# Kernel optimization log

Measured on AMD Instinct MI355X. Metric: run time of the kernel, lower is better.

The kernel has to match this reference:

```python
import jax, jax.numpy as jnp
import numpy as np

B, S, R, C = 1, 256, 256, 256   # batch, sequence_num, sequence_size, channel_size_msa
H, D = 8, 32                     # nhead, hidden_channel
EPS = 1e-5


def setup_inputs() -> dict:
    key = jax.random.key(0)
    ks = jax.random.split(key, 6)
    sd = 0.02
    return {
        "msa_repr": jax.random.normal(ks[0], (B, S, R, C), jnp.float32),
        "ln_w": jnp.ones((S,), jnp.float32),
        "ln_b": jnp.zeros((S,), jnp.float32),
        "Wq": jax.random.normal(ks[1], (C, H * D), jnp.float32) * sd,
        "Wk": jax.random.normal(ks[2], (C, H * D), jnp.float32) * sd,
        "Wv": jax.random.normal(ks[3], (C, H * D), jnp.float32) * sd,
        "Wg": jax.random.normal(ks[4], (C, H * D), jnp.float32) * sd,
        "bg": jnp.zeros((H * D,), jnp.float32),
        "Wo": jax.random.normal(ks[5], (H * D, C), jnp.float32) * sd,
        "bo": jnp.zeros((C,), jnp.float32),
    }


def reference(msa_repr, ln_w, ln_b, Wq, Wk, Wv, Wg, bg, Wo, bo):
    b, s, r, c = msa_repr.shape
    # [b, s, r, c] -> [b, r, s, c]: attention runs across sequences (column-wise)
    x = jnp.transpose(msa_repr, (0, 2, 1, 3))
    # LayerNorm over the s (sequence_num) axis, weight/bias indexed by s
    mu = jnp.mean(x, axis=2, keepdims=True)
    var = jnp.var(x, axis=2, keepdims=True)
    x = (x - mu) / jnp.sqrt(var + EPS)
    x = x * ln_w[None, None, :, None] + ln_b[None, None, :, None]
    x = x.reshape(b * r, s, c)  # flatten residue columns into batch

    q = (x @ Wq).reshape(b * r, s, H, D)
    k = (x @ Wk).reshape(b * r, s, H, D)
    v = (x @ Wv).reshape(b * r, s, H, D)
    g = jax.nn.sigmoid(x @ Wg + bg).reshape(b * r, s, H, D)

    scale = 1.0 / np.sqrt(D).astype(np.float32)
    logits = jnp.einsum('bihd,bjhd->bhij', q, k) * scale  # [(b r), H, s, s]
    attn = jax.nn.softmax(logits, axis=-1)
    out = jnp.einsum('bhij,bjhd->bihd', attn, v)           # [(b r), s, H, D]
    out = (g * out).reshape(b * r, s, H * D)
    out = out @ Wo + bo                                    # [(b r), s, c]
    out = out.reshape(b, r, s, c)
    return jnp.transpose(out, (0, 2, 1, 3))                # [b, s, r, c]
```

## Files before the change

kernel.cpp:

```cpp
#include <hip/hip_runtime.h>
#include <hip/hip_bf16.h>


using f32x4  = __attribute__((ext_vector_type(4))) float;
using bf16x8 = __attribute__((ext_vector_type(8))) short;

struct U4x { unsigned a0, a1, a2, a3; };
static_assert(sizeof(U4x) == sizeof(bf16x8), "frag size");

__device__ __forceinline__ f32x4 mfma16(bf16x8 a, bf16x8 b, f32x4 c){
  return __builtin_amdgcn_mfma_f32_16x16x32_bf16(a, b, c, 0, 0, 0);
}
__device__ __forceinline__ unsigned f2bf(float f){
  unsigned u = __builtin_bit_cast(unsigned, f);
  u += 0x7fffu + ((u >> 16) & 1u);
  return u >> 16;
}
__device__ __forceinline__ unsigned pk2(float lo, float hi){
  return f2bf(lo) | (f2bf(hi) << 16);
}
__device__ __forceinline__ bf16x8 mk_frag(unsigned a0, unsigned a1, unsigned a2, unsigned a3){
  U4x t{a0, a1, a2, a3};
  return __builtin_bit_cast(bf16x8, t);
}
__device__ __forceinline__ float sigm(float x){ return 1.f / (1.f + __expf(-x)); }

__device__ __forceinline__ int xaddr(int row, int cbyte){
  return (row << 9) + (cbyte ^ ((row & 15) << 4));
}
__device__ __forceinline__ bf16x8 lds_frag(const char* sm, int row, int cshort){
  return *(const bf16x8*)(sm + xaddr(row, cshort * 2));
}
__device__ __forceinline__ bf16x8 ldg_frag(const short* base, int row, int cshort){
  return *(const bf16x8*)(base + row * 256 + cshort);
}

__global__ __launch_bounds__(256) void prep_weights(
    const float* __restrict__ Wq, const float* __restrict__ Wk,
    const float* __restrict__ Wv, const float* __restrict__ Wg,
    const float* __restrict__ Wo, short* __restrict__ ws)
{
  const int n = blockIdx.x, t = threadIdx.x;
  ws[0*65536 + n*256 + t] = (short)f2bf(Wq[t*256 + n]);
  ws[1*65536 + n*256 + t] = (short)f2bf(Wk[t*256 + n]);
  ws[2*65536 + n*256 + t] = (short)f2bf(Wv[t*256 + n]);
  ws[3*65536 + n*256 + t] = (short)f2bf(Wg[t*256 + n]);
  ws[4*65536 + n*256 + t] = (short)f2bf(Wo[t*256 + n]);
}

__device__ __forceinline__ void build_x_tile_512(
    char* sm, const float* msa_r, const float* lnw, const float* lnb, int tid)
{
  float* muA = (float*)(sm + 131072);
  float* rsA = muA + 256;
  {
    float s0 = 0.f, s1 = 0.f;
    const int c = tid & 255, sh = tid >> 8;
    const float* p = msa_r + (sh * 128) * 65536 + c;
    #pragma unroll 8
    for (int i = 0; i < 128; i++){ float v = p[i * 65536]; s0 += v; s1 += v * v; }
    float* sb = (float*)sm;
    sb[tid] = s0; sb[512 + tid] = s1;
    __syncthreads();
    if (tid < 256){
      float tot = sb[tid] + sb[256 + tid];
      float sq  = sb[512 + tid] + sb[768 + tid];
      float mu  = tot * (1.f / 256.f);
      float var = fmaxf(sq * (1.f / 256.f) - mu * mu, 0.f);
      muA[tid] = mu; rsA[tid] = rsqrtf(var + 1e-5f);
    }
    __syncthreads();
  }
  {
    const int c0 = (tid & 31) * 8;
    float mu0[8], rs0[8];
    #pragma unroll
    for (int k = 0; k < 8; k++){ mu0[k] = muA[c0 + k]; rs0[k] = rsA[c0 + k]; }
    for (int itr = 0; itr < 16; itr++){
      const int s = itr * 16 + (tid >> 5);
      const float w = lnw[s], b = lnb[s];
      const float* rp = msa_r + s * 65536 + c0;
      f32x4 v0 = *(const f32x4*)rp;
      f32x4 v1 = *(const f32x4*)(rp + 4);
      U4x q{pk2((v0.x-mu0[0])*rs0[0]*w+b, (v0.y-mu0[1])*rs0[1]*w+b),
            pk2((v0.z-mu0[2])*rs0[2]*w+b, (v0.w-mu0[3])*rs0[3]*w+b),
            pk2((v1.x-mu0[4])*rs0[4]*w+b, (v1.y-mu0[5])*rs0[5]*w+b),
            pk2((v1.z-mu0[6])*rs0[6]*w+b, (v1.w-mu0[7])*rs0[7]*w+b)};
      *(U4x*)(sm + xaddr(s, c0 * 2)) = q;
    }
    __syncthreads();
  }
}

__global__ __launch_bounds__(512) void msa_qkvg(
    const float* __restrict__ msa, const float* __restrict__ lnw,
    const float* __restrict__ lnb, const float* __restrict__ bg,
    const short* __restrict__ wsW,
    uint4* __restrict__ kvF, uint2* __restrict__ qF, uint4* __restrict__ gF)
{
  extern __shared__ __align__(16) char sm[];
  const int r   = blockIdx.x;
  const int tid = threadIdx.x;
  build_x_tile_512(sm, msa + r * 256, lnw, lnb, tid);

  const int wid  = tid >> 6;
  const int lane = tid & 63;
  const int g = lane >> 4, c15 = lane & 15;
  const short* WqT = wsW;
  const short* WkT = wsW + 65536;
  const short* WvT = wsW + 2 * 65536;
  const short* WgT = wsW + 3 * 65536;
  const int hbase = wid * 32;
  const float bg0 = bg[hbase + c15], bg1 = bg[hbase + 16 + c15];
  const float scl = 0.17677669529663687f * 1.4426950408889634f;
  const f32x4 zz{0.f, 0.f, 0.f, 0.f};

  #pragma unroll 1
  for (int jt = 0; jt < 8; jt++){
    const int jb = jt * 32;
    f32x4 kt00=zz, kt01=zz, kt10=zz, kt11=zz;
    f32x4 va00=zz, va01=zz, va10=zz, va11=zz;
    #pragma unroll
    for (int kk = 0; kk < 8; kk++){
      const int cs = 32*kk + 8*g;
      bf16x8 wk0 = ldg_frag(WkT, hbase + c15,      cs);
      bf16x8 wk1 = ldg_frag(WkT, hbase + 16 + c15, cs);
      bf16x8 wv0 = ldg_frag(WvT, hbase + c15,      cs);
      bf16x8 wv1 = ldg_frag(WvT, hbase + 16 + c15, cs);
      bf16x8 bx0 = lds_frag(sm, jb + c15,      cs);
      bf16x8 bx1 = lds_frag(sm, jb + 16 + c15, cs);
      kt00 = mfma16(wk0, bx0, kt00);
      kt01 = mfma16(wk0, bx1, kt01);
      kt10 = mfma16(wk1, bx0, kt10);
      kt11 = mfma16(wk1, bx1, kt11);
      va00 = mfma16(bx0, wv0, va00);
      va01 = mfma16(bx0, wv1, va01);
      va10 = mfma16(bx1, wv0, va10);
      va11 = mfma16(bx1, wv1, va11);
    }
    const bf16x8 kf0 = mk_frag(pk2(kt00.x,kt00.y), pk2(kt00.z,kt00.w),
                               pk2(kt10.x,kt10.y), pk2(kt10.z,kt10.w));
    const bf16x8 kf1 = mk_frag(pk2(kt01.x,kt01.y), pk2(kt01.z,kt01.w),
                               pk2(kt11.x,kt11.y), pk2(kt11.z,kt11.w));
    const bf16x8 vf0 = mk_frag(pk2(va00.x,va00.y), pk2(va00.z,va00.w),
                               pk2(va10.x,va10.y), pk2(va10.z,va10.w));
    const bf16x8 vf1 = mk_frag(pk2(va01.x,va01.y), pk2(va01.z,va01.w),
                               pk2(va11.x,va11.y), pk2(va11.z,va11.w));
    const size_t kb = ((size_t)(r*64 + wid*8 + jt) * 4) * 64 + lane;
    kvF[kb      ] = __builtin_bit_cast(uint4, kf0);
    kvF[kb +  64] = __builtin_bit_cast(uint4, kf1);
    kvF[kb + 128] = __builtin_bit_cast(uint4, vf0);
    kvF[kb + 192] = __builtin_bit_cast(uint4, vf1);
  }

  #pragma unroll 1
  for (int dr = 0; dr < 2; dr++){
    bf16x8 wq[8];
    #pragma unroll
    for (int kk = 0; kk < 8; kk++) wq[kk] = ldg_frag(WqT, hbase + 16*dr + c15, 32*kk + 8*g);
    #pragma unroll 1
    for (int it = 0; it < 16; it++){
      f32x4 a = zz;
      #pragma unroll
      for (int kk = 0; kk < 8; kk++)
        a = mfma16(wq[kk], lds_frag(sm, it*16 + c15, 32*kk + 8*g), a);
      uint2 qv; qv.x = pk2(a.x*scl, a.y*scl); qv.y = pk2(a.z*scl, a.w*scl);
      qF[(((size_t)(r*8 + wid)*16 + it)*2 + dr)*64 + lane] = qv;
    }
  }

  #pragma unroll 1
  for (int dr = 0; dr < 2; dr++){
    bf16x8 wg[8];
    #pragma unroll
    for (int kk = 0; kk < 8; kk++) wg[kk] = ldg_frag(WgT, hbase + 16*dr + c15, 32*kk + 8*g);
    const float bgd = dr ? bg1 : bg0;
    #pragma unroll 1
    for (int it = 0; it < 16; it++){
      f32x4 a = zz;
      #pragma unroll
      for (int kk = 0; kk < 8; kk++)
        a = mfma16(lds_frag(sm, it*16 + c15, 32*kk + 8*g), wg[kk], a);
      f32x4 ga; ga.x = sigm(a.x + bgd); ga.y = sigm(a.y + bgd);
      ga.z = sigm(a.z + bgd); ga.w = sigm(a.w + bgd);
      gF[(((size_t)(r*8 + wid)*16 + it)*2 + dr)*64 + lane] = __builtin_bit_cast(uint4, ga);
    }
  }
}

__global__ __launch_bounds__(256) void msa_flash(
    const uint4* __restrict__ kvF, const uint2* __restrict__ qF,
    const uint4* __restrict__ gF, short* __restrict__ go)
{
  const int wid  = threadIdx.x >> 6;
  const int lane = threadIdx.x & 63;
  const int g = lane >> 4, c15 = lane & 15;
  const int w   = blockIdx.x * 4 + wid;
  const int r   = w >> 5;
  const int rem = w & 31;
  const int h   = rem >> 2;
  const int chq = rem & 3;
  const int hbase = h * 32;
  const int ib = chq * 64;
  const f32x4 zz{0.f, 0.f, 0.f, 0.f};

  bf16x8 bSq[4];
  #pragma unroll
  for (int nt = 0; nt < 4; nt++){
    const size_t qb = (((size_t)(r*8 + h)*16 + (ib >> 4) + nt)*2)*64 + lane;
    uint2 qlo = qF[qb], qhi = qF[qb + 64];
    bSq[nt] = mk_frag(qlo.x, qlo.y, qhi.x, qhi.y);
  }

  float l_[4];
  f32x4 o_[4][2];
  #pragma unroll
  for (int i2 = 0; i2 < 4; i2++){ l_[i2] = 0.f; o_[i2][0] = zz; o_[i2][1] = zz; }

  #pragma unroll 2
  for (int jt = 0; jt < 8; jt++){
    const size_t kb = ((size_t)(r*64 + h*8 + jt) * 4) * 64 + lane;
    const bf16x8 kf0 = __builtin_bit_cast(bf16x8, kvF[kb      ]);
    const bf16x8 kf1 = __builtin_bit_cast(bf16x8, kvF[kb +  64]);
    const bf16x8 vf0 = __builtin_bit_cast(bf16x8, kvF[kb + 128]);
    const bf16x8 vf1 = __builtin_bit_cast(bf16x8, kvF[kb + 192]);
    #pragma unroll
    for (int it = 0; it < 4; it++){
      f32x4 s0 = mfma16(kf0, bSq[it], zz);
      f32x4 s1 = mfma16(kf1, bSq[it], zz);
      float e0=exp2f(s0.x), e1=exp2f(s0.y), e2=exp2f(s0.z), e3=exp2f(s0.w);
      float e4=exp2f(s1.x), e5=exp2f(s1.y), e6=exp2f(s1.z), e7=exp2f(s1.w);
      l_[it] += ((e0+e1)+(e2+e3)) + ((e4+e5)+(e6+e7));
      bf16x8 aP = mk_frag(pk2(e0,e1), pk2(e2,e3), pk2(e4,e5), pk2(e6,e7));
      o_[it][0] = mfma16(aP, vf0, o_[it][0]);
      o_[it][1] = mfma16(aP, vf1, o_[it][1]);
    }
  }

  short* goR = go + (size_t)r * 65536;
  #pragma unroll
  for (int dr = 0; dr < 2; dr++){
    #pragma unroll
    for (int nt = 0; nt < 4; nt++){
      f32x4 ga = __builtin_bit_cast(f32x4,
          gF[(((size_t)(r*8 + h)*16 + (ib >> 4) + nt)*2 + dr)*64 + lane]);
      float lt = l_[nt];
      lt += __shfl_xor(lt, 16); lt += __shfl_xor(lt, 32);
      float inv[4];
      #pragma unroll
      for (int jj = 0; jj < 4; jj++) inv[jj] = 1.f / __shfl(lt, 4*g + jj);
      const f32x4 ov = o_[nt][dr];
      const unsigned w0 = pk2(ov[0]*inv[0]*ga.x, ov[1]*inv[1]*ga.y);
      const unsigned w1 = pk2(ov[2]*inv[2]*ga.z, ov[3]*inv[3]*ga.w);
      short* gp = goR + (ib + nt*16 + 4*g) * 256 + hbase + 16*dr + c15;
      gp[0]   = (short)(w0 & 0xffffu);
      gp[256] = (short)(w0 >> 16);
      gp[512] = (short)(w1 & 0xffffu);
      gp[768] = (short)(w1 >> 16);
    }
  }
}

__global__ __launch_bounds__(256) void out_proj(
    const short* __restrict__ go, const short* __restrict__ WoT,
    const float* __restrict__ bo, float* __restrict__ out)
{
  const int blk = blockIdx.x;
  const int r = blk >> 2, chunk = blk & 3;
  const int wid = threadIdx.x >> 6, lane = threadIdx.x & 63;
  const int g = lane >> 4, c15 = lane & 15;
  const int it = chunk * 4 + wid;
  const short* goR = go + (size_t)r * 65536;

  bf16x8 aGO[8];
  #pragma unroll
  for (int kk = 0; kk < 8; kk++) aGO[kk] = ldg_frag(goR, it*16 + c15, 32*kk + 8*g);
  #pragma unroll 2
  for (int ct = 0; ct < 16; ct++){
    f32x4 acc{0,0,0,0};
    #pragma unroll
    for (int kk = 0; kk < 8; kk++)
      acc = mfma16(aGO[kk], ldg_frag(WoT, ct*16 + c15, 32*kk + 8*g), acc);
    const float bov = bo[ct*16 + c15];
    const int i0 = it*16 + g*4;
    const int cc = ct*16 + c15;
    out[(i0 + 0) * 65536 + r * 256 + cc] = acc.x + bov;
    out[(i0 + 1) * 65536 + r * 256 + cc] = acc.y + bov;
    out[(i0 + 2) * 65536 + r * 256 + cc] = acc.z + bov;
    out[(i0 + 3) * 65536 + r * 256 + cc] = acc.w + bov;
  }
}

__global__ __launch_bounds__(512) void msa_attn_go(
    const float* __restrict__ msa, const float* __restrict__ lnw,
    const float* __restrict__ lnb, const float* __restrict__ bg,
    const short* __restrict__ wsW, short* __restrict__ go)
{
  extern __shared__ __align__(16) char sm[];
  const int r   = blockIdx.x;
  const int tid = threadIdx.x;
  build_x_tile_512(sm, msa + r * 256, lnw, lnb, tid);

  const int wid  = tid >> 6;
  const int lane = tid & 63;
  const int g = lane >> 4, c15 = lane & 15;
  const short* WqT = wsW;
  const short* WkT = wsW + 65536;
  const short* WvT = wsW + 2 * 65536;
  const short* WgT = wsW + 3 * 65536;
  const int hbase = wid * 32;
  const float bg0 = bg[hbase + c15], bg1 = bg[hbase + 16 + c15];
  const float scl = 0.17677669529663687f * 1.4426950408889634f;
  const f32x4 zz{0.f, 0.f, 0.f, 0.f};
  short* goR = go + r * 65536;

  #pragma unroll 1
  for (int chq = 0; chq < 4; chq++){
    const int ib = chq * 64;
    unsigned qTa[4][2], qTb[4][2];
    #pragma unroll
    for (int dr = 0; dr < 2; dr++){
      bf16x8 wq[8];
      #pragma unroll
      for (int kk = 0; kk < 8; kk++) wq[kk] = ldg_frag(WqT, hbase + 16*dr + c15, 32*kk + 8*g);
      #pragma unroll
      for (int nt = 0; nt < 4; nt++){
        f32x4 a = zz;
        #pragma unroll
        for (int kk = 0; kk < 8; kk++)
          a = mfma16(wq[kk], lds_frag(sm, ib + nt*16 + c15, 32*kk + 8*g), a);
        if (dr == 0){ qTa[nt][0] = pk2(a.x*scl, a.y*scl); qTa[nt][1] = pk2(a.z*scl, a.w*scl); }
        else        { qTb[nt][0] = pk2(a.x*scl, a.y*scl); qTb[nt][1] = pk2(a.z*scl, a.w*scl); }
      }
    }
    float l_[4];
    f32x4 o_[4][2];
    #pragma unroll
    for (int i2 = 0; i2 < 4; i2++){ l_[i2] = 0.f; o_[i2][0] = zz; o_[i2][1] = zz; }
    #pragma unroll 1
    for (int jt = 0; jt < 8; jt++){
      const int jb = jt * 32;
      f32x4 kt00=zz, kt01=zz, kt10=zz, kt11=zz;
      f32x4 va00=zz, va01=zz, va10=zz, va11=zz;
      #pragma unroll
      for (int kk = 0; kk < 8; kk++){
        const int cs = 32*kk + 8*g;
        bf16x8 wk0 = ldg_frag(WkT, hbase + c15,      cs);
        bf16x8 wk1 = ldg_frag(WkT, hbase + 16 + c15, cs);
        bf16x8 wv0 = ldg_frag(WvT, hbase + c15,      cs);
        bf16x8 wv1 = ldg_frag(WvT, hbase + 16 + c15, cs);
        bf16x8 bx0 = lds_frag(sm, jb + c15,      cs);
        bf16x8 bx1 = lds_frag(sm, jb + 16 + c15, cs);
        kt00 = mfma16(wk0, bx0, kt00);
        kt01 = mfma16(wk0, bx1, kt01);
        kt10 = mfma16(wk1, bx0, kt10);
        kt11 = mfma16(wk1, bx1, kt11);
        va00 = mfma16(bx0, wv0, va00);
        va01 = mfma16(bx0, wv1, va01);
        va10 = mfma16(bx1, wv0, va10);
        va11 = mfma16(bx1, wv1, va11);
      }
      const bf16x8 kf0 = mk_frag(pk2(kt00.x,kt00.y), pk2(kt00.z,kt00.w),
                                 pk2(kt10.x,kt10.y), pk2(kt10.z,kt10.w));
      const bf16x8 kf1 = mk_frag(pk2(kt01.x,kt01.y), pk2(kt01.z,kt01.w),
                                 pk2(kt11.x,kt11.y), pk2(kt11.z,kt11.w));
      const bf16x8 vf0 = mk_frag(pk2(va00.x,va00.y), pk2(va00.z,va00.w),
                                 pk2(va10.x,va10.y), pk2(va10.z,va10.w));
      const bf16x8 vf1 = mk_frag(pk2(va01.x,va01.y), pk2(va01.z,va01.w),
                                 pk2(va11.x,va11.y), pk2(va11.z,va11.w));
      #pragma unroll
      for (int it = 0; it < 4; it++){
        bf16x8 bS = mk_frag(qTa[it][0], qTa[it][1], qTb[it][0], qTb[it][1]);
        f32x4 s0 = mfma16(kf0, bS, zz);
        f32x4 s1 = mfma16(kf1, bS, zz);
        float e0=exp2f(s0.x), e1=exp2f(s0.y), e2=exp2f(s0.z), e3=exp2f(s0.w);
        float e4=exp2f(s1.x), e5=exp2f(s1.y), e6=exp2f(s1.z), e7=exp2f(s1.w);
        l_[it] += ((e0+e1)+(e2+e3)) + ((e4+e5)+(e6+e7));
        bf16x8 aP = mk_frag(pk2(e0,e1), pk2(e2,e3), pk2(e4,e5), pk2(e6,e7));
        o_[it][0] = mfma16(aP, vf0, o_[it][0]);
        o_[it][1] = mfma16(aP, vf1, o_[it][1]);
      }
    }
    #pragma unroll
    for (int dr = 0; dr < 2; dr++){
      const float bgd = dr ? bg1 : bg0;
      #pragma unroll
      for (int nt = 0; nt < 4; nt++){
        f32x4 a = zz;
        #pragma unroll
        for (int kk = 0; kk < 8; kk++)
          a = mfma16(lds_frag(sm, ib + nt*16 + c15, 32*kk + 8*g),
                     ldg_frag(WgT, hbase + 16*dr + c15, 32*kk + 8*g), a);
        float lt = l_[nt];
        lt += __shfl_xor(lt, 16); lt += __shfl_xor(lt, 32);
        float inv[4];
        #pragma unroll
        for (int jj = 0; jj < 4; jj++) inv[jj] = 1.f / __shfl(lt, 4*g + jj);
        const float ga0 = sigm(a.x + bgd), ga1 = sigm(a.y + bgd);
        const float ga2 = sigm(a.z + bgd), ga3 = sigm(a.w + bgd);
        const f32x4 ov = o_[nt][dr];
        const unsigned w0 = pk2(ov[0]*inv[0]*ga0, ov[1]*inv[1]*ga1);
        const unsigned w1 = pk2(ov[2]*inv[2]*ga2, ov[3]*inv[3]*ga3);
        short* gp = goR + (ib + nt*16 + 4*g) * 256 + hbase + 16*dr + c15;
        gp[0]   = (short)(w0 & 0xffffu);
        gp[256] = (short)(w0 >> 16);
        gp[512] = (short)(w1 & 0xffffu);
        gp[768] = (short)(w1 >> 16);
      }
    }
  }
}

extern "C" void kernel_launch(void* const* d_in, const int* in_sizes, int n_in,
                              void* d_out, int out_size, void* d_ws, size_t ws_size,
                              hipStream_t stream)
{
  (void)in_sizes; (void)n_in; (void)out_size;
  const float* msa = (const float*)d_in[0];
  const float* lnw = (const float*)d_in[1];
  const float* lnb = (const float*)d_in[2];
  const float* Wq  = (const float*)d_in[3];
  const float* Wk  = (const float*)d_in[4];
  const float* Wv  = (const float*)d_in[5];
  const float* Wg  = (const float*)d_in[6];
  const float* bg  = (const float*)d_in[7];
  const float* Wo  = (const float*)d_in[8];
  const float* bo  = (const float*)d_in[9];
  short* ws = (short*)d_ws;
  char* base = (char*)d_ws;

  prep_weights<<<256, 256, 0, stream>>>(Wq, Wk, Wv, Wg, Wo, ws);

  const size_t WB  = (size_t)5 * 65536 * 2;
  const size_t KVB = (size_t)256*8*8*4*64 * 16;
  const size_t QB  = (size_t)256*8*16*2*64 * 8;
  const size_t GB  = (size_t)256*8*16*2*64 * 16;
  const size_t GOB = (size_t)256*65536 * 2;
  const size_t need_big = WB + KVB + QB + GB + GOB;

  if (ws_size >= need_big){
    uint4* kvF = (uint4*)(base + WB);
    uint2* qF  = (uint2*)(base + WB + KVB);
    uint4* gF  = (uint4*)(base + WB + KVB + QB);
    short* goB = (short*)(base + WB + KVB + QB + GB);
    msa_qkvg <<<256, 512, 133120, stream>>>(msa, lnw, lnb, bg, ws, kvF, qF, gF);
    msa_flash<<<2048, 256, 0, stream>>>(kvF, qF, gF, goB);
    out_proj <<<1024, 256, 0, stream>>>(goB, ws + 4*65536, bo, (float*)d_out);
  } else {
    short* goB = (short*)(base + WB);
    msa_attn_go<<<256, 512, 133120, stream>>>(msa, lnw, lnb, bg, ws, goB);
    out_proj  <<<1024, 256, 0, stream>>>(goB, ws + 4*65536, bo, (float*)d_out);
  }
}
```

Before: 198.0 us.

## Fuse flash attention with output projection via shared-memory staging

Merges the attention kernel and the output-projection kernel into one launch. Each 512-thread block handles all 8 heads for a 64-row chunk of one residue column and writes the gated attention output into swizzled LDS instead of global memory. After a barrier, the same block multiplies that tile by Wo. This removes one kernel launch and a 32MB bf16 global round trip, but changes the block shape and occupancy of the attention phase and adds a block-wide sync.

```diff
diff --git a/kernel.cpp b/kernel.cpp
--- a/kernel.cpp
+++ b/kernel.cpp
@@ -33,6 +33,12 @@
 }
 __device__ __forceinline__ bf16x8 ldg_frag(const short* base, int row, int cshort){
   return *(const bf16x8*)(base + row * 256 + cshort);
+}
+__device__ __forceinline__ void store_go(char* sm, int i0, int hd, unsigned v0, unsigned v1){
+  *(short*)(sm + xaddr(i0 + 0, hd * 2)) = (short)(v0 & 0xffffu);
+  *(short*)(sm + xaddr(i0 + 1, hd * 2)) = (short)(v0 >> 16);
+  *(short*)(sm + xaddr(i0 + 2, hd * 2)) = (short)(v1 & 0xffffu);
+  *(short*)(sm + xaddr(i0 + 3, hd * 2)) = (short)(v1 >> 16);
 }
 
 __global__ __launch_bounds__(256) void prep_weights(
@@ -188,18 +194,18 @@
   }
 }
 
-__global__ __launch_bounds__(256) void msa_flash(
+__global__ __launch_bounds__(512) void msa_flash_proj(
     const uint4* __restrict__ kvF, const uint2* __restrict__ qF,
-    const uint4* __restrict__ gF, short* __restrict__ go)
-{
-  const int wid  = threadIdx.x >> 6;
-  const int lane = threadIdx.x & 63;
+    const uint4* __restrict__ gF,  const short* __restrict__ WoT,
+    const float* __restrict__ bo,  float* __restrict__ out)
+{
+  __shared__ __align__(16) char sm[32768];
+  const int tid  = threadIdx.x;
+  const int h    = tid >> 6;
+  const int lane = tid & 63;
   const int g = lane >> 4, c15 = lane & 15;
-  const int w   = blockIdx.x * 4 + wid;
-  const int r   = w >> 5;
-  const int rem = w & 31;
-  const int h   = rem >> 2;
-  const int chq = rem & 3;
+  const int blk = blockIdx.x;
+  const int r = blk >> 2, chq = blk & 3;
   const int hbase = h * 32;
   const int ib = chq * 64;
   const f32x4 zz{0.f, 0.f, 0.f, 0.f};
@@ -237,7 +243,6 @@
     }
   }
 
-  short* goR = go + (size_t)r * 65536;
   #pragma unroll
   for (int dr = 0; dr < 2; dr++){
     #pragma unroll
@@ -252,42 +257,30 @@
       const f32x4 ov = o_[nt][dr];
       const unsigned w0 = pk2(ov[0]*inv[0]*ga.x, ov[1]*inv[1]*ga.y);
       const unsigned w1 = pk2(ov[2]*inv[2]*ga.z, ov[3]*inv[3]*ga.w);
-      short* gp = goR + (ib + nt*16 + 4*g) * 256 + hbase + 16*dr + c15;
-      gp[0]   = (short)(w0 & 0xffffu);
-      gp[256] = (short)(w0 >> 16);
-      gp[512] = (short)(w1 & 0xffffu);
-      gp[768] = (short)(w1 >> 16);
-    }
-  }
-}
-
-__global__ __launch_bounds__(256) void out_proj(
-    const short* __restrict__ go, const short* __restrict__ WoT,
-    const float* __restrict__ bo, float* __restrict__ out)
-{
-  const int blk = blockIdx.x;
-  const int r = blk >> 2, chunk = blk & 3;
-  const int wid = threadIdx.x >> 6, lane = threadIdx.x & 63;
-  const int g = lane >> 4, c15 = lane & 15;
-  const int it = chunk * 4 + wid;
-  const short* goR = go + (size_t)r * 65536;
-
+      store_go(sm, nt*16 + 4*g, hbase + 16*dr + c15, w0, w1);
+    }
+  }
+  __syncthreads();
+
+  const int it2 = h & 3;
+  const int cth = (h >> 2) * 8;
   bf16x8 aGO[8];
   #pragma unroll
-  for (int kk = 0; kk < 8; kk++) aGO[kk] = ldg_frag(goR, it*16 + c15, 32*kk + 8*g);
+  for (int kk = 0; kk < 8; kk++) aGO[kk] = lds_frag(sm, it2*16 + c15, 32*kk + 8*g);
   #pragma unroll 2
-  for (int ct = 0; ct < 16; ct++){
-    f32x4 acc{0,0,0,0};
+  for (int c8 = 0; c8 < 8; c8++){
+    const int ct = cth + c8;
+    f32x4 acc = zz;
     #pragma unroll
     for (int kk = 0; kk < 8; kk++)
       acc = mfma16(aGO[kk], ldg_frag(WoT, ct*16 + c15, 32*kk + 8*g), acc);
     const float bov = bo[ct*16 + c15];
-    const int i0 = it*16 + g*4;
+    const int i0 = ib + it2*16 + g*4;
     const int cc = ct*16 + c15;
-    out[(i0 + 0) * 65536 + r * 256 + cc] = acc.x + bov;
-    out[(i0 + 1) * 65536 + r * 256 + cc] = acc.y + bov;
-    out[(i0 + 2) * 65536 + r * 256 + cc] = acc.z + bov;
-    out[(i0 + 3) * 65536 + r * 256 + cc] = acc.w + bov;
+    out[(size_t)(i0 + 0) * 65536 + r * 256 + cc] = acc.x + bov;
+    out[(size_t)(i0 + 1) * 65536 + r * 256 + cc] = acc.y + bov;
+    out[(size_t)(i0 + 2) * 65536 + r * 256 + cc] = acc.z + bov;
+    out[(size_t)(i0 + 3) * 65536 + r * 256 + cc] = acc.w + bov;
   }
 }
 
@@ -411,6 +404,36 @@
   }
 }
 
+__global__ __launch_bounds__(256) void out_proj(
+    const short* __restrict__ go, const short* __restrict__ WoT,
+    const float* __restrict__ bo, float* __restrict__ out)
+{
+  const int blk = blockIdx.x;
+  const int r = blk >> 2, chunk = blk & 3;
+  const int wid = threadIdx.x >> 6, lane = threadIdx.x & 63;
+  const int g = lane >> 4, c15 = lane & 15;
+  const int it = chunk * 4 + wid;
+  const short* goR = go + (size_t)r * 65536;
+
+  bf16x8 aGO[8];
+  #pragma unroll
+  for (int kk = 0; kk < 8; kk++) aGO[kk] = ldg_frag(goR, it*16 + c15, 32*kk + 8*g);
+  #pragma unroll 2
+  for (int ct = 0; ct < 16; ct++){
+    f32x4 acc{0,0,0,0};
+    #pragma unroll
+    for (int kk = 0; kk < 8; kk++)
+      acc = mfma16(aGO[kk], ldg_frag(WoT, ct*16 + c15, 32*kk + 8*g), acc);
+    const float bov = bo[ct*16 + c15];
+    const int i0 = it*16 + g*4;
+    const int cc = ct*16 + c15;
+    out[(i0 + 0) * 65536 + r * 256 + cc] = acc.x + bov;
+    out[(i0 + 1) * 65536 + r * 256 + cc] = acc.y + bov;
+    out[(i0 + 2) * 65536 + r * 256 + cc] = acc.z + bov;
+    out[(i0 + 3) * 65536 + r * 256 + cc] = acc.w + bov;
+  }
+}
+
 extern "C" void kernel_launch(void* const* d_in, const int* in_sizes, int n_in,
                               void* d_out, int out_size, void* d_ws, size_t ws_size,
                               hipStream_t stream)
@@ -435,17 +458,14 @@
   const size_t KVB = (size_t)256*8*8*4*64 * 16;
   const size_t QB  = (size_t)256*8*16*2*64 * 8;
   const size_t GB  = (size_t)256*8*16*2*64 * 16;
-  const size_t GOB = (size_t)256*65536 * 2;
-  const size_t need_big = WB + KVB + QB + GB + GOB;
+  const size_t need_big = WB + KVB + QB + GB;
 
   if (ws_size >= need_big){
     uint4* kvF = (uint4*)(base + WB);
     uint2* qF  = (uint2*)(base + WB + KVB);
     uint4* gF  = (uint4*)(base + WB + KVB + QB);
-    short* goB = (short*)(base + WB + KVB + QB + GB);
-    msa_qkvg <<<256, 512, 133120, stream>>>(msa, lnw, lnb, bg, ws, kvF, qF, gF);
-    msa_flash<<<2048, 256, 0, stream>>>(kvF, qF, gF, goB);
-    out_proj <<<1024, 256, 0, stream>>>(goB, ws + 4*65536, bo, (float*)d_out);
+    msa_qkvg      <<<256, 512, 133120, stream>>>(msa, lnw, lnb, bg, ws, kvF, qF, gF);
+    msa_flash_proj<<<1024, 512, 0, stream>>>(kvF, qF, gF, ws + 4*65536, bo, (float*)d_out);
   } else {
     short* goB = (short*)(base + WB);
     msa_attn_go<<<256, 512, 133120, stream>>>(msa, lnw, lnb, bg, ws, goB);
```

After: 184.7 us. 1.07x faster.
